# Optimization experiments

Hardware: AMD Instinct MI355X
Metric: run time of the kernel (lower is better)

The kernel has to match this reference:

```python
import jax, jax.numpy as jnp
import numpy as np

C = 64      # in_channels
H = 32      # hidden_size per direction
K = 8       # kernel_size
L = 4       # num_layers
EPS = 1e-5


def _sru_dir(x, W, v, b, reverse):
    # x: (T, N, in); one SRU direction.
    if reverse:
        x = x[::-1]
    U = x @ W                                   # (T, N, 4H): [candidate z, f_pre, r_pre, highway x']
    z, fp, rp, xp = jnp.split(U, 4, axis=-1)
    vf, vr = jnp.split(v, 2)
    bf, br = jnp.split(b, 2)

    def step(c, inp):
        z_t, fp_t, rp_t, xp_t = inp
        f = jax.nn.sigmoid(fp_t + vf * c + bf)
        r = jax.nn.sigmoid(rp_t + vr * c + br)
        c_new = f * c + (1.0 - f) * z_t
        h = r * c_new + (1.0 - r) * xp_t
        return c_new, h

    c0 = jnp.zeros((x.shape[1], H), x.dtype)
    _, h = jax.lax.scan(step, c0, (z, fp, rp, xp))
    if reverse:
        h = h[::-1]
    return h


def _sru(x, W0, Wr, v, b):
    # Bidirectional multi-layer SRU. x: (T, N, C*K) -> (T, N, 2H)
    Ws = [W0] + [Wr[i] for i in range(Wr.shape[0])]
    h = x
    for l in range(L):
        hf = _sru_dir(h, Ws[l][0], v[l, 0], b[l, 0], False)
        hb = _sru_dir(h, Ws[l][1], v[l, 1], b[l, 1], True)
        h = jnp.concatenate([hf, hb], axis=-1)
    return h


def setup_inputs() -> dict:
    key = jax.random.key(0)
    ks = jax.random.split(key, 8)
    B, Fdim, Tdim = 2, 128, 250
    s = 0.05
    x = jax.random.normal(ks[0], (B, C, Fdim, Tdim), jnp.float32)
    gamma = jnp.ones((C,), jnp.float32)
    beta = jnp.zeros((C,), jnp.float32)
    W0 = jax.random.normal(ks[1], (2, C * K, 4 * H), jnp.float32) * s       # layer 0, 2 dirs
    Wr = jax.random.normal(ks[2], (L - 1, 2, 2 * H, 4 * H), jnp.float32) * s  # layers 1..3
    v = jax.random.normal(ks[3], (L, 2, 2 * H), jnp.float32) * s            # recurrent gate vectors
    b = jnp.zeros((L, 2, 2 * H), jnp.float32)                               # gate biases
    wct = jax.random.normal(ks[4], (2 * H, C, K), jnp.float32) * s          # ConvTranspose1d (in,out,k)
    bct = jnp.zeros((C,), jnp.float32)
    return {"x": x, "gamma": gamma, "beta": beta, "W0": W0, "Wr": Wr,
            "v": v, "b": b, "wct": wct, "bct": bct}


def reference(x, gamma, beta, W0, Wr, v, b, wct, bct):
    x = jnp.swapaxes(x, -1, -2)                 # [B, C, T, F]
    res = x
    B, Cc, T, F = x.shape
    # GroupNorm(num_groups=1): normalize over (C,T,F) per sample, per-channel affine.
    mean = jnp.mean(x, axis=(1, 2, 3), keepdims=True)
    var = jnp.var(x, axis=(1, 2, 3), keepdims=True)
    xn = (x - mean) * jax.lax.rsqrt(var + EPS)
    xn = xn * gamma[None, :, None, None] + beta[None, :, None, None]
    # -> (B*F, C, T), then unfold over T with window K (channel-major block layout).
    xu = jnp.transpose(xn, (0, 3, 1, 2)).reshape(B * F, Cc, T)
    Tn = T - K + 1
    win = jnp.stack([xu[:, :, k:k + Tn] for k in range(K)], axis=2)   # (N, C, K, Tn)
    win = win.reshape(B * F, Cc * K, Tn)
    s = jnp.transpose(win, (2, 0, 1))           # (Tn, N, C*K)
    h = _sru(s, W0, Wr, v, b)                   # (Tn, N, 2H)
    y = jnp.transpose(h, (1, 2, 0))             # (N, 2H, Tn)
    # ConvTranspose1d stride 1 == full correlation with flipped kernel.
    w_conv = jnp.transpose(wct, (1, 0, 2))[:, :, ::-1]                # (out, in, k)
    y = jax.lax.conv_general_dilated(y, w_conv, (1,), [(K - 1, K - 1)],
                                     dimension_numbers=("NCH", "OIH", "NCH"))
    y = y + bct[None, :, None]                  # (N, C, T)
    y = y.reshape(B, F, Cc, T)
    y = jnp.transpose(y, (0, 2, 3, 1))          # [B, C, T, F]
    y = y + res
    return jnp.swapaxes(y, -1, -2)              # back to [B, C, F, T]
```

## Files before the change

### kernel.cpp

```cpp
#include <hip/hip_runtime.h>
#include <math.h>

#define Tt 250
#define TnN 243
#define Nn 256
#define EPS_ 1e-5f
#define LOG2E 1.44269504f

typedef unsigned short u16;
typedef __bf16 bf16x8 __attribute__((ext_vector_type(8)));
typedef float f32x4 __attribute__((ext_vector_type(4)));

__device__ __forceinline__ u16 f2bf(float f) {
    unsigned u = __builtin_bit_cast(unsigned, f);
    u += 0x7FFFu + ((u >> 16) & 1u);
    return (u16)(u >> 16);
}
__device__ __forceinline__ float bf2f(u16 s) {
    unsigned u = ((unsigned)s) << 16;
    return __builtin_bit_cast(float, u);
}
__device__ __forceinline__ float hw_exp2(float x) {
    return __builtin_amdgcn_exp2f(x);
}

__device__ __forceinline__ void async_load16(const void* g, void* l) {
    __builtin_amdgcn_global_load_lds(
        (const __attribute__((address_space(1))) unsigned int*)g,
        (__attribute__((address_space(3))) unsigned int*)l, 16, 0, 0);
}

__device__ __forceinline__ void dma72g(const u16* gsrc, int rstride, u16* ldst, int nseg,
                                       int w, int lane, int nw) {
    for (int seg = w; seg < nseg; seg += nw) {
        int c9 = seg * 64 + lane;
        int row = c9 / 9, sub = c9 - row * 9;
        const u16* src = (sub < 8) ? &gsrc[row * rstride + sub * 8] : gsrc;
        async_load16(src, ldst + seg * 512);
    }
}

template<int D>
__device__ __forceinline__ void chain_run(u16* Zr, u16* Fr, float kf, float bf_) {
    bf16x8 z8 = *(const bf16x8*)&Zr[D ? 240 : 0];
    bf16x8 f8 = *(const bf16x8*)&Fr[D ? 240 : 0];
    float c = 0.f;
    for (int grp = 0; grp < 31; ++grp) {
        int gb = D ? (30 - grp) * 8 : grp * 8;
        bf16x8 zn = z8, fn = f8;
        if (grp < 30) {
            int gbn = D ? (29 - grp) * 8 : (grp + 1) * 8;
            zn = *(const bf16x8*)&Zr[gbn];
            fn = *(const bf16x8*)&Fr[gbn];
        }
        bf16x8 co;
        #pragma unroll
        for (int k = 0; k < 8; ++k) {
            const int idx = D ? (7 - k) : k;
            int t = gb + idx;
            float uz = (float)z8[idx];
            float af = -LOG2E * ((float)f8[idx] + bf_);
            float xe = fmaf(kf, c, af);
            float fg = __builtin_amdgcn_rcpf(1.f + hw_exp2(xe));
            float cn = fmaf(fg, c - uz, uz);
            bool ok = (t < TnN);
            if (ok) c = cn;
            co[idx] = ok ? (__bf16)c : (__bf16)0.f;
        }
        *(bf16x8*)&Zr[gb] = co;
        z8 = zn; f8 = fn;
    }
}

__global__ __launch_bounds__(256) void k_prep(const float* __restrict__ x,
                                              const float* __restrict__ W0,
                                              const float* __restrict__ Wr,
                                              const float* __restrict__ wct,
                                              float* __restrict__ stats,
                                              u16* __restrict__ W0k,
                                              u16* __restrict__ Wrt,
                                              u16* __restrict__ Wcto) {
    __shared__ float ls[4], ls2[4];
    const int bx = blockIdx.x, tid = threadIdx.x;
    if (bx < 832) {
        int idx = bx * 256 + tid;
        if (idx < 131072) {
            int k = idx >> 14, j = (idx >> 6) & 255, c = idx & 63;
            int d = j >> 7, ck = c * 8 + k;
            W0k[idx] = f2bf(W0[((size_t)d * 512 + ck) * 128 + (j & 127)]);
        } else if (idx < 180224) {
            int r = idx - 131072;
            int i = r & 63, j = (r >> 6) & 255, lidx = r >> 14;
            Wrt[r] = f2bf(Wr[(size_t)(lidx * 2 + (j >> 7)) * 8192 + i * 128 + (j & 127)]);
        } else {
            int r = idx - 180224;
            int o = r >> 9; int k = r & 511; int kk = k >> 6, ci = k & 63;
            Wcto[r] = f2bf(wct[(size_t)ci * 512 + o * 8 + kk]);
        }
    } else {
        const int sb = bx - 832;
        const int b = sb >> 7;
        const float4* xb = (const float4*)(x + (size_t)b * 64 * 128 * Tt);
        const int n4 = 64 * 128 * Tt / 4;
        float s = 0.f, s2 = 0.f;
        for (int i = (sb & 127) * 256 + tid; i < n4; i += 128 * 256) {
            float4 vv = xb[i];
            s  += vv.x + vv.y + vv.z + vv.w;
            s2 += vv.x * vv.x + vv.y * vv.y + vv.z * vv.z + vv.w * vv.w;
        }
        for (int off = 32; off; off >>= 1) {
            s  += __shfl_down(s, off);
            s2 += __shfl_down(s2, off);
        }
        int lane = tid & 63, w = tid >> 6;
        if (lane == 0) { ls[w] = s; ls2[w] = s2; }
        __syncthreads();
        if (tid == 0) {
            float a = 0.f, a2 = 0.f;
            for (int i = 0; i < 4; i++) { a += ls[i]; a2 += ls2[i]; }
            atomicAdd(&stats[b * 2 + 0], a);
            atomicAdd(&stats[b * 2 + 1], a2);
        }
    }
}

__global__ __launch_bounds__(512) void k_norm(const float* __restrict__ x, const float* __restrict__ stats,
                       const float* __restrict__ gamma, const float* __restrict__ beta,
                       u16* __restrict__ xbt) {
    __shared__ u16 lt[64 * 260];
    const int n = blockIdx.x, tid = threadIdx.x;
    const int b = n >> 7, f = n & 127;
    const float inv = 1.0f / (float)(64 * 128 * Tt);
    float mean = stats[b * 2 + 0] * inv;
    float var  = stats[b * 2 + 1] * inv - mean * mean;
    float rstd = rsqrtf(var + EPS_);
    const int c = tid >> 3, vq = tid & 7;
    const float gm = gamma[c] * rstd;
    const float bt = beta[c] - mean * gm;
    const float* xr = x + ((size_t)(b * 64 + c) * 128 + f) * Tt;
    #pragma unroll
    for (int j = 0; j < 16; ++j) {
        int t0 = vq * 2 + j * 16;
        unsigned pv = 0u;
        if (t0 < Tt) {
            float2 xv = *(const float2*)&xr[t0];
            pv = (unsigned)f2bf(fmaf(xv.x, gm, bt)) | ((unsigned)f2bf(fmaf(xv.y, gm, bt)) << 16);
        }
        *(unsigned*)&lt[c * 260 + t0] = pv;
    }
    __syncthreads();
    const int cg = tid & 7, tq = tid >> 3;
    #pragma unroll
    for (int it = 0; it < 4; ++it) {
        int t = it * 64 + tq;
        u16 tmp[8];
        #pragma unroll
        for (int jj = 0; jj < 8; ++jj) tmp[jj] = lt[(cg * 8 + jj) * 260 + t];
        uint4 o;
        o.x = (unsigned)tmp[0] | ((unsigned)tmp[1] << 16);
        o.y = (unsigned)tmp[2] | ((unsigned)tmp[3] << 16);
        o.z = (unsigned)tmp[4] | ((unsigned)tmp[5] << 16);
        o.w = (unsigned)tmp[6] | ((unsigned)tmp[7] << 16);
        *(uint4*)&xbt[(size_t)n * 16384 + t * 64 + cg * 8] = o;
    }
}

#define HS0 0
#define ZT0 19008
#define FT0 34880
#define BM0 50752
#define SH_U16 81856
__global__ __launch_bounds__(1024) void k_tail(const u16* __restrict__ XbT,
                                               const u16* __restrict__ W0k,
                                               const u16* __restrict__ Wrt,
                                               const u16* __restrict__ Wc,
                                               const float* __restrict__ v,
                                               const float* __restrict__ bbias,
                                               const float* __restrict__ bct,
                                               const float* __restrict__ x,
                                               float* __restrict__ out) {
    __shared__ __align__(16) u16 sh[SH_U16];
    u16* Hs = sh + HS0;
    u16* ZT = sh + ZT0;
    u16* FT = sh + FT0;
    u16* Bm = sh + BM0;
    const int tid = threadIdx.x;
    const int n = blockIdx.x;
    const int lane = tid & 63, w = tid >> 6;
    const int ml = lane & 15, q = lane >> 4;
    const int b = n >> 7, f = n & 127;
    const int t0 = w * 16 + q * 4;

    for (int lay = 0; lay < 4; ++lay) {
        f32x4 acc[16];
        #pragma unroll
        for (int nt = 0; nt < 16; ++nt) acc[nt] = (f32x4){0.f, 0.f, 0.f, 0.f};

        if (lay == 0) {
            const u16* Xn = XbT + (size_t)n * 16384;
            u16* Bb0 = sh + ZT0;
            u16* Bb1 = Bm;
            dma72g(Xn, 64, Hs, 36, w, lane, 16);
            dma72g(W0k, 64, Bb0, 36, w, lane, 16);
            __syncthreads();
            #pragma unroll
            for (int k = 0; k < 8; ++k) {
                u16* Bl = (k & 1) ? Bb1 : Bb0;
                if (k < 7)
                    dma72g(W0k + (size_t)(k + 1) * 16384, 64, (k & 1) ? Bb0 : Bb1, 36, w, lane, 16);
                #pragma unroll
                for (int c2 = 0; c2 < 2; ++c2) {
                    int c0 = c2 * 32;
                    bf16x8 af = *(const bf16x8*)&Hs[(w * 16 + ml + k) * 72 + c0 + q * 8];
                    #pragma unroll
                    for (int nt = 0; nt < 16; ++nt) {
                        bf16x8 bfr = *(const bf16x8*)&Bl[(nt * 16 + ml) * 72 + c0 + q * 8];
                        acc[nt] = __builtin_amdgcn_mfma_f32_16x16x32_bf16(af, bfr, acc[nt], 0, 0, 0);
                    }
                }
                __syncthreads();
            }
        } else {
            #pragma unroll
            for (int c2 = 0; c2 < 2; ++c2) {
                int c0 = c2 * 32;
                bf16x8 af = *(const bf16x8*)&Hs[(w * 16 + ml + 7) * 72 + c0 + q * 8];
                #pragma unroll
                for (int nt = 0; nt < 16; ++nt) {
                    bf16x8 bfr = *(const bf16x8*)&Bm[(nt * 16 + ml) * 72 + c0 + q * 8];
                    acc[nt] = __builtin_amdgcn_mfma_f32_16x16x32_bf16(af, bfr, acc[nt], 0, 0, 0);
                }
            }
        }

        if (t0 < TnN) {
            bool vec = (t0 + 4 <= TnN);
            #pragma unroll
            for (int d2 = 0; d2 < 2; ++d2)
                #pragma unroll
                for (int j = 0; j < 4; ++j) {
                    int nt = d2 * 8 + j;
                    int g2 = j >> 1, hi = j & 1, hh = hi * 16 + ml;
                    u16* P = (g2 ? FT : ZT) + (d2 * 32 + hh) * 248;
                    if (vec) {
                        uint2 pv;
                        pv.x = (unsigned)f2bf(acc[nt][0]) | ((unsigned)f2bf(acc[nt][1]) << 16);
                        pv.y = (unsigned)f2bf(acc[nt][2]) | ((unsigned)f2bf(acc[nt][3]) << 16);
                        *(uint2*)&P[t0] = pv;
                    } else {
                        #pragma unroll
                        for (int r = 0; r < 4; ++r) {
                            int t = t0 + r;
                            if (t < TnN) P[t] = f2bf(acc[nt][r]);
                        }
                    }
                }
        }
        __syncthreads();

        if (lay < 3) {
            dma72g(Wrt + (size_t)lay * 16384, 64, Bm, 36, w, lane, 16);
        } else {
            #pragma unroll
            for (int i = 0; i < 4; ++i)
                dma72g(Wc + i * 64, 512, Bm + i * 4608, 9, w, lane, 16);
        }

        const float* vv = v + (size_t)(lay * 2) * 64;
        const float* bv = bbias + (size_t)(lay * 2) * 64;

        if (w < 2 && lane < 32) {
            const int d = w, h = lane;
            const float vf = vv[d * 64 + h], bf_ = bv[d * 64 + h];
            const float kf = -LOG2E * vf;
            u16* Zr = &ZT[(d * 32 + h) * 248];
            u16* Fr = &FT[(d * 32 + h) * 248];
            if (d == 0) chain_run<0>(Zr, Fr, kf, bf_);
            else        chain_run<1>(Zr, Fr, kf, bf_);
        }
        __syncthreads();

        if (lay == 0) {
            for (int i = tid; i < 21 * 72; i += 1024) {
                int r = i / 72, ci = i - r * 72;
                int row = r < 7 ? r : (TnN + r);
                Hs[row * 72 + ci] = 0;
            }
        }
        #pragma unroll
        for (int d2 = 0; d2 < 2; ++d2)
            #pragma unroll
            for (int hi = 0; hi < 2; ++hi) {
                int hh = hi * 16 + ml;
                float vr_ = vv[d2 * 64 + 32 + hh], br_ = bv[d2 * 64 + 32 + hh];
                float kr = -LOG2E * vr_;
                const u16* Cr = &ZT[(d2 * 32 + hh) * 248];
                f32x4 rp = acc[d2 * 8 + 4 + hi];
                f32x4 xp = acc[d2 * 8 + 6 + hi];
                #pragma unroll
                for (int r = 0; r < 4; ++r) {
                    int t = t0 + r;
                    if (t < TnN) {
                        float ct = bf2f(Cr[t]);
                        float cpr;
                        if (d2 == 0) cpr = (t == 0) ? 0.f : bf2f(Cr[t - 1]);
                        else         cpr = (t == TnN - 1) ? 0.f : bf2f(Cr[t + 1]);
                        float xr = fmaf(kr, cpr, -LOG2E * (rp[r] + br_));
                        float rg = __builtin_amdgcn_rcpf(1.f + hw_exp2(xr));
                        float hv = fmaf(rg, ct - xp[r], xp[r]);
                        Hs[(t + 7) * 72 + d2 * 32 + hh] = f2bf(hv);
                    }
                }
            }
        __syncthreads();
    }

    {
        u16* T47 = sh + ZT0;
        float* Cf = (float*)(sh + 37440);
        f32x4 cacc[4] = {};
        #pragma unroll
        for (int i = 0; i < 4; ++i)
            dma72g(Wc + (4 + i) * 64, 512, T47 + i * 4608, 9, w, lane, 16);
        #pragma unroll
        for (int m = 0; m < 8; ++m) {
            if (m == 4) __syncthreads();
            const u16* Bl = (m < 4) ? (Bm + m * 4608) : (T47 + (m - 4) * 4608);
            #pragma unroll
            for (int c2 = 0; c2 < 2; ++c2) {
                int ci0 = c2 * 32;
                bf16x8 af = *(const bf16x8*)&Hs[(w * 16 + ml - m + 7) * 72 + ci0 + q * 8];
                #pragma unroll
                for (int nt = 0; nt < 4; ++nt) {
                    bf16x8 bfv = *(const bf16x8*)&Bl[(nt * 16 + ml) * 72 + ci0 + q * 8];
                    cacc[nt] = __builtin_amdgcn_mfma_f32_16x16x32_bf16(af, bfv, cacc[nt], 0, 0, 0);
                }
            }
        }
        __syncthreads();
        float bc[4];
        #pragma unroll
        for (int nt = 0; nt < 4; ++nt) bc[nt] = bct[nt * 16 + ml];
        #pragma unroll
        for (int r = 0; r < 4; ++r) {
            int t = t0 + r;
            if (t < Tt) {
                #pragma unroll
                for (int nt = 0; nt < 4; ++nt)
                    Cf[t * 68 + nt * 16 + ml] = cacc[nt][r] + bc[nt];
            }
        }
        __syncthreads();
        {
            const int sub = tid & 15;
            const int o = tid >> 4;
            const float* xrow = x + ((size_t)(b * 64 + o) * 128 + f) * Tt;
            float* orow = out + ((size_t)(b * 64 + o) * 128 + f) * Tt;
            #pragma unroll
            for (int it = 0; it < 8; ++it) {
                int j = it * 32 + sub * 2;
                if (j < Tt) {
                    float2 xv = *(const float2*)&xrow[j];
                    float2 ov;
                    ov.x = Cf[j * 68 + o] + xv.x;
                    ov.y = Cf[(j + 1) * 68 + o] + xv.y;
                    *(float2*)&orow[j] = ov;
                }
            }
        }
    }
}

extern "C" void kernel_launch(void* const* d_in, const int* in_sizes, int n_in,
                              void* d_out, int out_size, void* d_ws, size_t ws_size,
                              hipStream_t stream) {
    (void)in_sizes; (void)n_in; (void)out_size; (void)ws_size;
    const float* x     = (const float*)d_in[0];
    const float* gamma = (const float*)d_in[1];
    const float* beta  = (const float*)d_in[2];
    const float* W0    = (const float*)d_in[3];
    const float* Wr    = (const float*)d_in[4];
    const float* v     = (const float*)d_in[5];
    const float* bb    = (const float*)d_in[6];
    const float* wct   = (const float*)d_in[7];
    const float* bct   = (const float*)d_in[8];
    float* out = (float*)d_out;

    char* base = (char*)d_ws;
    float* stats = (float*)base;
    u16* W0k  = (u16*)(base + 256);
    u16* Wrt  = (u16*)(base + 256 + 262144);
    u16* Wcto = (u16*)(base + 256 + 262144 + 98304);
    u16* XbT  = (u16*)(base + 426240);

    hipMemsetAsync(stats, 0, 32, stream);
    k_prep<<<dim3(1088), 256, 0, stream>>>(x, W0, Wr, wct, stats, W0k, Wrt, Wcto);
    k_norm<<<dim3(256), 512, 0, stream>>>(x, stats, gamma, beta, XbT);
    k_tail<<<dim3(256), 1024, 0, stream>>>(XbT, W0k, Wrt, Wcto, v, bb, bct, x, out);
}
```

Measured before the change: 188.5 us.

## Fuse stats reduction and normalization into one cooperative kernel with grid sync

Merges k_prep and k_norm into a single cooperative launch of 1024 blocks. Blocks now write per-block partial sums instead of using atomics, a grid-wide sync separates the phases, and each block then normalizes and transposes a quarter of one (b,f) row. This removes one kernel launch, the memset and the atomics, at the cost of a grid barrier and the requirement that all 1024 blocks be co-resident. Stats blocks drop from 256 to 192, which leaves fewer workers for the reduction.

```diff
diff --git a/kernel.cpp b/kernel.cpp
--- a/kernel.cpp
+++ b/kernel.cpp
@@ -1,4 +1,5 @@
 #include <hip/hip_runtime.h>
+#include <hip/hip_cooperative_groups.h>
 #include <math.h>
 
 #define Tt 250
@@ -76,11 +77,15 @@
                                               const float* __restrict__ W0,
                                               const float* __restrict__ Wr,
                                               const float* __restrict__ wct,
+                                              const float* __restrict__ gamma,
+                                              const float* __restrict__ beta,
                                               float* __restrict__ stats,
                                               u16* __restrict__ W0k,
                                               u16* __restrict__ Wrt,
-                                              u16* __restrict__ Wcto) {
-    __shared__ float ls[4], ls2[4];
+                                              u16* __restrict__ Wcto,
+                                              u16* __restrict__ xbt) {
+    __shared__ float ls[4], ls2[4], sm2[2];
+    __shared__ u16 lt[64 * 68];
     const int bx = blockIdx.x, tid = threadIdx.x;
     if (bx < 832) {
         int idx = bx * 256 + tid;
@@ -99,11 +104,12 @@
         }
     } else {
         const int sb = bx - 832;
-        const int b = sb >> 7;
+        const int b = sb >= 96 ? 1 : 0;
+        const int sbb = sb - b * 96;
         const float4* xb = (const float4*)(x + (size_t)b * 64 * 128 * Tt);
         const int n4 = 64 * 128 * Tt / 4;
         float s = 0.f, s2 = 0.f;
-        for (int i = (sb & 127) * 256 + tid; i < n4; i += 128 * 256) {
+        for (int i = sbb * 256 + tid; i < n4; i += 96 * 256) {
             float4 vv = xb[i];
             s  += vv.x + vv.y + vv.z + vv.w;
             s2 += vv.x * vv.x + vv.y * vv.y + vv.z * vv.z + vv.w * vv.w;
@@ -118,50 +124,66 @@
         if (tid == 0) {
             float a = 0.f, a2 = 0.f;
             for (int i = 0; i < 4; i++) { a += ls[i]; a2 += ls2[i]; }
-            atomicAdd(&stats[b * 2 + 0], a);
-            atomicAdd(&stats[b * 2 + 1], a2);
-        }
-    }
-}
-
-__global__ __launch_bounds__(512) void k_norm(const float* __restrict__ x, const float* __restrict__ stats,
-                       const float* __restrict__ gamma, const float* __restrict__ beta,
-                       u16* __restrict__ xbt) {
-    __shared__ u16 lt[64 * 260];
-    const int n = blockIdx.x, tid = threadIdx.x;
-    const int b = n >> 7, f = n & 127;
-    const float inv = 1.0f / (float)(64 * 128 * Tt);
-    float mean = stats[b * 2 + 0] * inv;
-    float var  = stats[b * 2 + 1] * inv - mean * mean;
-    float rstd = rsqrtf(var + EPS_);
-    const int c = tid >> 3, vq = tid & 7;
-    const float gm = gamma[c] * rstd;
-    const float bt = beta[c] - mean * gm;
-    const float* xr = x + ((size_t)(b * 64 + c) * 128 + f) * Tt;
-    #pragma unroll
-    for (int j = 0; j < 16; ++j) {
-        int t0 = vq * 2 + j * 16;
-        unsigned pv = 0u;
-        if (t0 < Tt) {
-            float2 xv = *(const float2*)&xr[t0];
-            pv = (unsigned)f2bf(fmaf(xv.x, gm, bt)) | ((unsigned)f2bf(fmaf(xv.y, gm, bt)) << 16);
-        }
-        *(unsigned*)&lt[c * 260 + t0] = pv;
-    }
-    __syncthreads();
-    const int cg = tid & 7, tq = tid >> 3;
-    #pragma unroll
-    for (int it = 0; it < 4; ++it) {
-        int t = it * 64 + tq;
-        u16 tmp[8];
-        #pragma unroll
-        for (int jj = 0; jj < 8; ++jj) tmp[jj] = lt[(cg * 8 + jj) * 260 + t];
-        uint4 o;
-        o.x = (unsigned)tmp[0] | ((unsigned)tmp[1] << 16);
-        o.y = (unsigned)tmp[2] | ((unsigned)tmp[3] << 16);
-        o.z = (unsigned)tmp[4] | ((unsigned)tmp[5] << 16);
-        o.w = (unsigned)tmp[6] | ((unsigned)tmp[7] << 16);
-        *(uint4*)&xbt[(size_t)n * 16384 + t * 64 + cg * 8] = o;
+            stats[4 + sb * 2]     = a;
+            stats[4 + sb * 2 + 1] = a2;
+        }
+    }
+    cooperative_groups::this_grid().sync();
+
+    {
+        const int n = bx >> 2, quarter = bx & 3;
+        const int b2 = n >> 7, f = n & 127;
+        if (tid < 64) {
+            float a = 0.f, a2 = 0.f;
+            for (int p = tid; p < 96; p += 64) {
+                a  += stats[4 + (b2 * 96 + p) * 2];
+                a2 += stats[4 + (b2 * 96 + p) * 2 + 1];
+            }
+            for (int off = 32; off; off >>= 1) {
+                a  += __shfl_down(a, off);
+                a2 += __shfl_down(a2, off);
+            }
+            if (tid == 0) { sm2[0] = a; sm2[1] = a2; }
+        }
+        __syncthreads();
+        const float inv = 1.0f / (float)(64 * 128 * Tt);
+        float mean = sm2[0] * inv;
+        float var  = sm2[1] * inv - mean * mean;
+        float rstd = rsqrtf(var + EPS_);
+        const int c = tid >> 2, vq = tid & 3;
+        float gm = gamma[c] * rstd;
+        float bt = beta[c] - mean * gm;
+        const float* xr = x + ((size_t)(b2 * 64 + c) * 128 + f) * Tt;
+        #pragma unroll
+        for (int j = 0; j < 4; ++j) {
+            int tl = vq * 16 + j * 4;
+            int tg = quarter * 64 + tl;
+            uint2 pv = {0u, 0u};
+            if (tg + 4 <= Tt) {
+                float4 xv = *(const float4*)&xr[tg];
+                pv.x = (unsigned)f2bf(fmaf(xv.x, gm, bt)) | ((unsigned)f2bf(fmaf(xv.y, gm, bt)) << 16);
+                pv.y = (unsigned)f2bf(fmaf(xv.z, gm, bt)) | ((unsigned)f2bf(fmaf(xv.w, gm, bt)) << 16);
+            } else if (tg < Tt) {
+                float2 xv2 = *(const float2*)&xr[tg];
+                pv.x = (unsigned)f2bf(fmaf(xv2.x, gm, bt)) | ((unsigned)f2bf(fmaf(xv2.y, gm, bt)) << 16);
+            }
+            *(uint2*)&lt[c * 68 + tl] = pv;
+        }
+        __syncthreads();
+        #pragma unroll
+        for (int it = 0; it < 2; ++it) {
+            int task = it * 256 + tid;
+            int tloc = task >> 3, cgp = task & 7;
+            u16 tmp[8];
+            #pragma unroll
+            for (int jj = 0; jj < 8; ++jj) tmp[jj] = lt[(cgp * 8 + jj) * 68 + tloc];
+            uint4 o;
+            o.x = (unsigned)tmp[0] | ((unsigned)tmp[1] << 16);
+            o.y = (unsigned)tmp[2] | ((unsigned)tmp[3] << 16);
+            o.z = (unsigned)tmp[4] | ((unsigned)tmp[5] << 16);
+            o.w = (unsigned)tmp[6] | ((unsigned)tmp[7] << 16);
+            *(uint4*)&xbt[(size_t)n * 16384 + (quarter * 64 + tloc) * 64 + cgp * 8] = o;
+        }
     }
 }
 
@@ -388,13 +410,13 @@
 
     char* base = (char*)d_ws;
     float* stats = (float*)base;
-    u16* W0k  = (u16*)(base + 256);
-    u16* Wrt  = (u16*)(base + 256 + 262144);
-    u16* Wcto = (u16*)(base + 256 + 262144 + 98304);
-    u16* XbT  = (u16*)(base + 426240);
-
-    hipMemsetAsync(stats, 0, 32, stream);
-    k_prep<<<dim3(1088), 256, 0, stream>>>(x, W0, Wr, wct, stats, W0k, Wrt, Wcto);
-    k_norm<<<dim3(256), 512, 0, stream>>>(x, stats, gamma, beta, XbT);
+    u16* W0k  = (u16*)(base + 2048);
+    u16* Wrt  = (u16*)(base + 2048 + 262144);
+    u16* Wcto = (u16*)(base + 2048 + 262144 + 98304);
+    u16* XbT  = (u16*)(base + 2048 + 262144 + 98304 + 65536);
+
+    void* args[] = {(void*)&x, (void*)&W0, (void*)&Wr, (void*)&wct, (void*)&gamma, (void*)&beta,
+                    (void*)&stats, (void*)&W0k, (void*)&Wrt, (void*)&Wcto, (void*)&XbT};
+    hipLaunchCooperativeKernel((const void*)k_prep, dim3(1024), dim3(256), args, 0, stream);
     k_tail<<<dim3(256), 1024, 0, stream>>>(XbT, W0k, Wrt, Wcto, v, bb, bct, x, out);
 }
```

Result: slower. 326.6 us (+73.3%).
